# Kernel optimization log

Hardware: AMD Instinct MI355X
Metric: run time of the kernel (lower is better)

Reference implementation:

```python
import jax, jax.numpy as jnp
import numpy as np

NS, NT = 4000, 4096
E_S, E_T = 64000, 65536
D_IN, D_H, N_LAYERS = 128, 256, 3
SINK_ITERS = 10
EPS = 1e-10
ALPHA = 20.0


def scatter_mean(vals, idx, n):
    # torch_geometric aggr='mean': sum then divide by count (0 where count==0)
    s = jax.ops.segment_sum(vals, idx, num_segments=n)
    c = jax.ops.segment_sum(jnp.ones((idx.shape[0],), vals.dtype), idx, num_segments=n)
    return s / jnp.maximum(c, 1.0)[:, None]


def rel_cnn(x, edge_index, layers, final_w, final_b):
    # RelCNN(batch_norm=False, cat=True, lin=True), eval mode (dropout off)
    src, dst = edge_index[0], edge_index[1]
    n = x.shape[0]
    xs = [x]
    h = x
    for (w1, w2, wr, br) in layers:
        out1 = scatter_mean((h @ w1)[src], dst, n)  # source->target mean agg
        out2 = scatter_mean((h @ w2)[dst], src, n)  # target->source mean agg
        h = jax.nn.relu(h @ wr + br + out1 + out2)  # RelConv: root + out1 + out2
        xs.append(h)
    return jnp.concatenate(xs, axis=-1) @ final_w + final_b


def sinkhorn(S):
    # Sinkhorn(max_iter=10, eps=1e-10) with dummy_row=True, exp=True, alpha=20
    ns, nt = S.shape  # ns <= nt: pad dummy rows set to eps
    pad = jnp.full((nt - ns, nt), EPS, S.dtype)
    s = jnp.concatenate([S, pad], axis=0) + EPS
    s = jnp.exp(ALPHA * s)
    for i in range(SINK_ITERS):
        if i % 2 == 1:  # row normalization
            s = s / s.sum(axis=1, keepdims=True)
        else:           # column normalization
            s = s / s.sum(axis=0, keepdims=True)
    return s[:ns, :]  # drop dummy rows


def l2norm(x):
    return x / jnp.maximum(jnp.linalg.norm(x, axis=1, keepdims=True), 1e-12)


def setup_inputs() -> dict:
    key = jax.random.key(0)
    ks = jax.random.split(key, 20)
    d = {
        'x_s': jax.random.normal(ks[0], (NS, D_IN), jnp.float32),
        'x_t': jax.random.normal(ks[1], (NT, D_IN), jnp.float32),
        'edges': jax.random.randint(ks[2], (2, E_S), 0, NS, jnp.int32),
        'edget': jax.random.randint(ks[3], (2, E_T), 0, NT, jnp.int32),
    }
    k = 4
    fan = D_IN
    for l in range(N_LAYERS):
        sc = 1.0 / np.sqrt(fan)
        d[f'W1_{l}'] = jax.random.normal(ks[k], (fan, D_H), jnp.float32) * sc; k += 1
        d[f'W2_{l}'] = jax.random.normal(ks[k], (fan, D_H), jnp.float32) * sc; k += 1
        d[f'Wr_{l}'] = jax.random.normal(ks[k], (fan, D_H), jnp.float32) * sc; k += 1
        d[f'br_{l}'] = jax.random.normal(ks[k], (D_H,), jnp.float32) * 0.01; k += 1
        fan = D_H
    fin = D_IN + N_LAYERS * D_H
    d['final_w'] = jax.random.normal(ks[k], (fin, D_H), jnp.float32) * (0.01 / np.sqrt(fin)); k += 1
    d['final_b'] = jax.random.normal(ks[k], (D_H,), jnp.float32) * 0.001
    return d


def reference(x_s, x_t, edges, edget,
              W1_0, W2_0, Wr_0, br_0,
              W1_1, W2_1, Wr_1, br_1,
              W1_2, W2_2, Wr_2, br_2,
              final_w, final_b):
    layers = [(W1_0, W2_0, Wr_0, br_0), (W1_1, W2_1, Wr_1, br_1), (W1_2, W2_2, Wr_2, br_2)]
    h_s = rel_cnn(x_s, edges, layers, final_w, final_b)   # [NS, D_H]
    h_t = rel_cnn(x_t, edget, layers, final_w, final_b)   # [NT, D_H]
    match = l2norm(h_s) @ l2norm(h_t).T                   # [NS, NT]
    return sinkhorn(match)
```

## Files before the change

kernel.cpp:

```cpp
#include <hip/hip_runtime.h>
#include <hip/hip_bf16.h>

#define NS_N 4000
#define NT_N 4096
#define NTOT 8096
#define ES_E 64000
#define ET_E 65536
#define ETOT 129536
#define D_IN 128
#define D_H 256
#define CAT_D 896
#define TMP_D 768
#define NDUM (NT_N - NS_N)
#define ALPHA_F 20.0f
#define EPS_F 1e-10f

typedef __attribute__((ext_vector_type(8))) short bf16x8;
typedef __attribute__((ext_vector_type(4))) float f32x4;

__device__ inline short f2bf(float v) {
    __hip_bfloat16 b = __float2bfloat16(v);
    return *reinterpret_cast<short*>(&b);
}
__device__ inline float bf2f(short s) {
    __hip_bfloat16 b = *reinterpret_cast<__hip_bfloat16*>(&s);
    return __bfloat162float(b);
}
__device__ inline void splitf(float v, short& hi, short& lo) {
    hi = f2bf(v);
    lo = f2bf(v - bf2f(hi));
}

typedef __attribute__((address_space(1))) const char gas_t;
typedef __attribute__((address_space(3))) char las_t;
__device__ inline void gload16(const short* g, short* l) {
    __builtin_amdgcn_global_load_lds((gas_t*)g, (las_t*)l, 16, 0, 0);
}

template<int EPI>
__global__ __launch_bounds__(256) void mfma_gemm_kernel(
    const short* __restrict__ Ahi, const short* __restrict__ Alo,
    const short* __restrict__ Bhi, const short* __restrict__ Blo,
    const float* __restrict__ bias, float* __restrict__ C,
    int M, int N, int K, int lda, int ldb, int ldc)
{
    __shared__ short sAh[128 * 32];
    __shared__ short sAl[128 * 32];
    __shared__ short sBh[128 * 32];
    __shared__ short sBl[128 * 32];
    const int bm = blockIdx.x * 128;
    const int bn = blockIdx.y * 128;
    const int t = threadIdx.x;
    const int lane = t & 63, wv = t >> 6;
    const int wr = wv >> 1, wc = wv & 1;
    const int lr = lane & 15, lg = lane >> 4;

    f32x4 acc[4][4];
    #pragma unroll
    for (int i = 0; i < 4; ++i)
        #pragma unroll
        for (int j = 0; j < 4; ++j) {
            f32x4 z = {0.f, 0.f, 0.f, 0.f};
            acc[i][j] = z;
        }

    const int srow = lane >> 2, sseg = (lane & 3) * 8;

    for (int k0 = 0; k0 < K; k0 += 32) {
        auto stage = [&](const short* src, short* dst, int rowbase, int ld, int maxrow) {
            #pragma unroll
            for (int q = 0; q < 8; ++q) {
                int gr = min(rowbase + q * 16 + srow, maxrow);
                gload16(src + (size_t)gr * ld + k0 + sseg, dst + q * 512);
            }
        };
        if (wv == 0)      stage(Ahi, sAh, bm, lda, M - 1);
        else if (wv == 1) stage(Alo, sAl, bm, lda, M - 1);
        else if (wv == 2) stage(Bhi, sBh, bn, ldb, N - 1);
        else              stage(Blo, sBl, bn, ldb, N - 1);
        __syncthreads();

        bf16x8 ah[4], al[4], bh[4], bl[4];
        #pragma unroll
        for (int i = 0; i < 4; ++i) {
            int oa = (wr * 64 + i * 16 + lr) * 32 + lg * 8;
            ah[i] = *reinterpret_cast<const bf16x8*>(&sAh[oa]);
            al[i] = *reinterpret_cast<const bf16x8*>(&sAl[oa]);
            int ob = (wc * 64 + i * 16 + lr) * 32 + lg * 8;
            bh[i] = *reinterpret_cast<const bf16x8*>(&sBh[ob]);
            bl[i] = *reinterpret_cast<const bf16x8*>(&sBl[ob]);
        }
        #pragma unroll
        for (int i = 0; i < 4; ++i)
            #pragma unroll
            for (int j = 0; j < 4; ++j) {
                acc[i][j] = __builtin_amdgcn_mfma_f32_16x16x32_bf16(ah[i], bh[j], acc[i][j], 0, 0, 0);
                acc[i][j] = __builtin_amdgcn_mfma_f32_16x16x32_bf16(ah[i], bl[j], acc[i][j], 0, 0, 0);
                acc[i][j] = __builtin_amdgcn_mfma_f32_16x16x32_bf16(al[i], bh[j], acc[i][j], 0, 0, 0);
            }
        __syncthreads();
    }
    #pragma unroll
    for (int i = 0; i < 4; ++i) {
        #pragma unroll
        for (int j = 0; j < 4; ++j) {
            int col = bn + wc * 64 + j * 16 + lr;
            #pragma unroll
            for (int r = 0; r < 4; ++r) {
                int row = bm + wr * 64 + i * 16 + lg * 4 + r;
                if (row < M) {
                    float v = acc[i][j][r];
                    if (EPI == 1) v += bias[col];
                    if (EPI == 2) v = expf(ALPHA_F * (v + EPS_F));
                    C[(size_t)row * ldc + col] = v;
                }
            }
        }
    }
}

__global__ void wsplit3_kernel(const float* __restrict__ W1, const float* __restrict__ W2,
                               const float* __restrict__ Wr, short* __restrict__ WThi,
                               short* __restrict__ WTlo, int K)
{
    int idx = blockIdx.x * 256 + threadIdx.x;
    if (idx < K * TMP_D) {
        int k = idx / TMP_D, c = idx % TMP_D;
        float v = (c < 256) ? W1[k * 256 + c]
                : (c < 512) ? W2[k * 256 + (c - 256)]
                            : Wr[k * 256 + (c - 512)];
        short hi, lo;
        splitf(v, hi, lo);
        WThi[(size_t)c * K + k] = hi;
        WTlo[(size_t)c * K + k] = lo;
    }
}

__global__ void wsplitT_kernel(const float* __restrict__ W, short* __restrict__ WThi,
                               short* __restrict__ WTlo, int K, int Nw)
{
    int idx = blockIdx.x * 256 + threadIdx.x;
    if (idx < K * Nw) {
        int k = idx / Nw, n = idx % Nw;
        short hi, lo;
        splitf(W[idx], hi, lo);
        WThi[(size_t)n * K + k] = hi;
        WTlo[(size_t)n * K + k] = lo;
    }
}

__global__ void count2_kernel(const int* __restrict__ es, const int* __restrict__ et,
                              int* __restrict__ cin, int* __restrict__ cout)
{
    int e = blockIdx.x * 256 + threadIdx.x;
    int dir = blockIdx.y;
    int* cnt = dir ? cout : cin;
    if (e < ES_E) {
        int key = dir ? es[e] : es[e + ES_E];
        atomicAdd(&cnt[key], 1);
    } else if (e < ETOT) {
        int e2 = e - ES_E;
        int key = dir ? et[e2] : et[e2 + ET_E];
        atomicAdd(&cnt[key + NS_N], 1);
    }
}

__global__ __launch_bounds__(256) void scan2_kernel(const int* __restrict__ cin,
                                                    const int* __restrict__ cout,
                                                    int* __restrict__ rpin, int* __restrict__ rpout,
                                                    int* __restrict__ curin, int* __restrict__ curout)
{
    const int* cnt = blockIdx.x ? cout : cin;
    int* rowptr = blockIdx.x ? rpout : rpin;
    int* cur = blockIdx.x ? curout : curin;
    __shared__ int sums[256];
    const int t = threadIdx.x;
    const int per = (NTOT + 255) / 256;
    const int lo = t * per, hi = min((t + 1) * per, NTOT);
    int s = 0;
    for (int i = lo; i < hi; ++i) s += cnt[i];
    sums[t] = s;
    __syncthreads();
    for (int off = 1; off < 256; off <<= 1) {
        int v = (t >= off) ? sums[t - off] : 0;
        __syncthreads();
        sums[t] += v;
        __syncthreads();
    }
    int base = (t == 0) ? 0 : sums[t - 1];
    for (int i = lo; i < hi; ++i) { rowptr[i] = base; cur[i] = base; base += cnt[i]; }
    if (t == 255) rowptr[NTOT] = base;
}

__global__ void fill2_kernel(const int* __restrict__ es, const int* __restrict__ et,
                             int* __restrict__ curin, int* __restrict__ curout,
                             int* __restrict__ ciin, int* __restrict__ ciout)
{
    int e = blockIdx.x * 256 + threadIdx.x;
    int dir = blockIdx.y;
    int* cur = dir ? curout : curin;
    int* ci = dir ? ciout : ciin;
    int key, val, off;
    if (e < ES_E) {
        key = dir ? es[e] : es[e + ES_E];
        val = dir ? es[e + ES_E] : es[e];
        off = 0;
    } else if (e < ETOT) {
        int e2 = e - ES_E;
        key = dir ? et[e2] : et[e2 + ET_E];
        val = dir ? et[e2 + ET_E] : et[e2];
        off = NS_N;
    } else return;
    int pos = atomicAdd(&cur[key + off], 1);
    ci[pos] = val + off;
}

__global__ void copy_x_kernel(const float* __restrict__ xs, const float* __restrict__ xt,
                              short* __restrict__ CAThi, short* __restrict__ CATlo)
{
    int i = blockIdx.x, d = threadIdx.x;
    float v = (i < NS_N) ? xs[(size_t)i * D_IN + d] : xt[(size_t)(i - NS_N) * D_IN + d];
    short hi, lo;
    splitf(v, hi, lo);
    CAThi[(size_t)i * CAT_D + d] = hi;
    CATlo[(size_t)i * CAT_D + d] = lo;
}

__global__ __launch_bounds__(256) void gather_combine_kernel(
    const float* __restrict__ TMP,
    const int* __restrict__ rp_in, const int* __restrict__ ci_in,
    const int* __restrict__ rp_out, const int* __restrict__ ci_out,
    const float* __restrict__ br, short* __restrict__ CAThi, short* __restrict__ CATlo,
    int catoff)
{
    int node = blockIdx.x * 4 + (threadIdx.x >> 6);
    if (node >= NTOT) return;
    int d = (threadIdx.x & 63) * 4;

    float4 a1 = make_float4(0.f, 0.f, 0.f, 0.f);
    int b0 = rp_in[node], e0 = rp_in[node + 1];
    for (int e = b0; e < e0; ++e) {
        const float4 v = *reinterpret_cast<const float4*>(&TMP[(size_t)ci_in[e] * TMP_D + d]);
        a1.x += v.x; a1.y += v.y; a1.z += v.z; a1.w += v.w;
    }
    float s1 = 1.f / (float)max(e0 - b0, 1);

    float4 a2 = make_float4(0.f, 0.f, 0.f, 0.f);
    int b1 = rp_out[node], e1 = rp_out[node + 1];
    for (int e = b1; e < e1; ++e) {
        const float4 v = *reinterpret_cast<const float4*>(&TMP[(size_t)ci_out[e] * TMP_D + 256 + d]);
        a2.x += v.x; a2.y += v.y; a2.z += v.z; a2.w += v.w;
    }
    float s2 = 1.f / (float)max(e1 - b1, 1);

    const float4 rt = *reinterpret_cast<const float4*>(&TMP[(size_t)node * TMP_D + 512 + d]);
    const float4 bb = *reinterpret_cast<const float4*>(&br[d]);
    float o[4];
    o[0] = fmaxf(rt.x + bb.x + a1.x * s1 + a2.x * s2, 0.f);
    o[1] = fmaxf(rt.y + bb.y + a1.y * s1 + a2.y * s2, 0.f);
    o[2] = fmaxf(rt.z + bb.z + a1.z * s1 + a2.z * s2, 0.f);
    o[3] = fmaxf(rt.w + bb.w + a1.w * s1 + a2.w * s2, 0.f);
    short h[4], l[4];
    #pragma unroll
    for (int q = 0; q < 4; ++q) splitf(o[q], h[q], l[q]);
    *reinterpret_cast<short4*>(&CAThi[(size_t)node * CAT_D + catoff + d]) = make_short4(h[0], h[1], h[2], h[3]);
    *reinterpret_cast<short4*>(&CATlo[(size_t)node * CAT_D + catoff + d]) = make_short4(l[0], l[1], l[2], l[3]);
}

__global__ __launch_bounds__(256) void l2norm_kernel(const float* __restrict__ in,
                                                     short* __restrict__ outhi,
                                                     short* __restrict__ outlo, int N)
{
    int row = blockIdx.x * 4 + (threadIdx.x >> 6);
    if (row >= N) return;
    int d = (threadIdx.x & 63) * 4;
    float4 v = *reinterpret_cast<const float4*>(&in[(size_t)row * D_H + d]);
    float s = v.x * v.x + v.y * v.y + v.z * v.z + v.w * v.w;
    #pragma unroll
    for (int off = 32; off; off >>= 1) s += __shfl_xor(s, off);
    float inv = 1.f / fmaxf(sqrtf(s), 1e-12f);
    float o[4] = {v.x * inv, v.y * inv, v.z * inv, v.w * inv};
    short h[4], l[4];
    #pragma unroll
    for (int q = 0; q < 4; ++q) splitf(o[q], h[q], l[q]);
    *reinterpret_cast<short4*>(&outhi[(size_t)row * D_H + d]) = make_short4(h[0], h[1], h[2], h[3]);
    *reinterpret_cast<short4*>(&outlo[(size_t)row * D_H + d]) = make_short4(l[0], l[1], l[2], l[3]);
}

template<bool FIRST>
__global__ __launch_bounds__(256) void colsum_kernel(
    const float* __restrict__ s0, const float* __restrict__ r, float* __restrict__ tsum)
{
    int j4 = blockIdx.x * 256 + threadIdx.x;
    int i0 = blockIdx.y * 32;
    int iend = min(i0 + 32, NS_N);
    float4 s = make_float4(0.f, 0.f, 0.f, 0.f);
    for (int i = i0; i < iend; ++i) {
        float ri = FIRST ? 1.f : r[i];
        const float4 v = *reinterpret_cast<const float4*>(&s0[(size_t)i * NT_N + j4 * 4]);
        s.x += ri * v.x; s.y += ri * v.y; s.z += ri * v.z; s.w += ri * v.w;
    }
    atomicAdd(&tsum[j4 * 4 + 0], s.x);
    atomicAdd(&tsum[j4 * 4 + 1], s.y);
    atomicAdd(&tsum[j4 * 4 + 2], s.z);
    atomicAdd(&tsum[j4 * 4 + 3], s.w);
}

template<bool FIRST, bool FUSE_OUT>
__global__ __launch_bounds__(256) void rowsum_kernel(
    const float* __restrict__ s0, const float* __restrict__ tsum,
    const float* __restrict__ rdR, float* __restrict__ rdW,
    float* __restrict__ r, float* __restrict__ tsumNext,
    float* __restrict__ out, float dummyv)
{
    int i = blockIdx.x;
    int t = threadIdx.x;
    if (i < 16) tsumNext[i * 256 + t] = 0.f;
    float rdv = FIRST ? 1.f : rdR[0];
    float dd = (float)NDUM * dummyv * rdv;
    float s = 0.f;
    if (i < NS_N) {
        for (int j4 = t; j4 < NT_N / 4; j4 += 256) {
            const float4 v = *reinterpret_cast<const float4*>(&s0[(size_t)i * NT_N + j4 * 4]);
            const float4 ts = *reinterpret_cast<const float4*>(&tsum[j4 * 4]);
            s += v.x / (ts.x + dd) + v.y / (ts.y + dd) + v.z / (ts.z + dd) + v.w / (ts.w + dd);
        }
    } else {
        for (int j = t; j < NT_N; j += 256) s += 1.f / (tsum[j] + dd);
    }
    #pragma unroll
    for (int off = 32; off; off >>= 1) s += __shfl_xor(s, off);
    __shared__ float ws[4];
    __shared__ float ri_sh;
    if ((t & 63) == 0) ws[t >> 6] = s;
    __syncthreads();
    if (t == 0) {
        float tot = ws[0] + ws[1] + ws[2] + ws[3];
        if (i < NS_N) { r[i] = 1.f / tot; ri_sh = 1.f / tot; }
        else rdW[0] = 1.f / (dummyv * tot);
    }
    if (FUSE_OUT) {
        __syncthreads();
        if (i < NS_N) {
            float ri = ri_sh;
            for (int j4 = t; j4 < NT_N / 4; j4 += 256) {
                const float4 v = *reinterpret_cast<const float4*>(&s0[(size_t)i * NT_N + j4 * 4]);
                const float4 ts = *reinterpret_cast<const float4*>(&tsum[j4 * 4]);
                float4 o = make_float4(ri * v.x / (ts.x + dd), ri * v.y / (ts.y + dd),
                                       ri * v.z / (ts.z + dd), ri * v.w / (ts.w + dd));
                *reinterpret_cast<float4*>(&out[(size_t)i * NT_N + j4 * 4]) = o;
            }
        }
    }
}

extern "C" void kernel_launch(void* const* d_in, const int* in_sizes, int n_in,
                              void* d_out, int out_size, void* d_ws, size_t ws_size,
                              hipStream_t stream)
{
    const float* x_s = (const float*)d_in[0];
    const float* x_t = (const float*)d_in[1];
    const int* edges = (const int*)d_in[2];
    const int* edget = (const int*)d_in[3];
    const float* W1[3] = {(const float*)d_in[4], (const float*)d_in[8], (const float*)d_in[12]};
    const float* W2[3] = {(const float*)d_in[5], (const float*)d_in[9], (const float*)d_in[13]};
    const float* Wr[3] = {(const float*)d_in[6], (const float*)d_in[10], (const float*)d_in[14]};
    const float* br[3] = {(const float*)d_in[7], (const float*)d_in[11], (const float*)d_in[15]};
    const float* final_w = (const float*)d_in[16];
    const float* final_b = (const float*)d_in[17];
    float* out = (float*)d_out;

    float* W = (float*)d_ws;
    size_t off = 0;
    float* S0 = W + off;  off += (size_t)NS_N * NT_N;
    float* TMP = W + off; off += (size_t)NTOT * TMP_D;
    short* CAThi = (short*)(W + off); off += (size_t)NTOT * CAT_D / 2;
    short* CATlo = (short*)(W + off); off += (size_t)NTOT * CAT_D / 2;
    const int fan[3] = {D_IN, D_H, D_H};
    short* WThi[3]; short* WTlo[3];
    for (int l = 0; l < 3; ++l) {
        WThi[l] = (short*)(W + off); off += (size_t)TMP_D * fan[l] / 2;
        WTlo[l] = (short*)(W + off); off += (size_t)TMP_D * fan[l] / 2;
    }
    short* WFhi = (short*)(W + off); off += (size_t)D_H * CAT_D / 2;
    short* WFlo = (short*)(W + off); off += (size_t)D_H * CAT_D / 2;
    float* RVEC = W + off; off += NS_N;
    float* RD   = W + off; off += 8;
    float* TSA  = W + off; off += NT_N;
    int* CNT_IN  = (int*)(W + off); off += NTOT;
    int* CNT_OUT = (int*)(W + off); off += NTOT;
    float* TSB  = W + off; off += NT_N;
    int* RP_IN   = (int*)(W + off); off += NTOT + 1;
    int* RP_OUT  = (int*)(W + off); off += NTOT + 3;
    int* CUR_IN  = (int*)(W + off); off += NTOT;
    int* CUR_OUT = (int*)(W + off); off += NTOT;
    int* CI_IN   = (int*)(W + off); off += ETOT;
    int* CI_OUT  = (int*)(W + off); off += ETOT;
    float* HFIN = TMP;
    short* HNhi = (short*)(TMP + (size_t)NTOT * D_H);
    short* HNlo = (short*)(TMP + (size_t)NTOT * D_H + (size_t)NTOT * D_H / 2);

    const int cat_off[4] = {0, 128, 384, 640};

    hipMemsetAsync(TSA, 0, (NT_N + 2 * NTOT) * sizeof(int), stream);

    for (int l = 0; l < 3; ++l)
        wsplit3_kernel<<<(fan[l] * TMP_D + 255) / 256, 256, 0, stream>>>(
            W1[l], W2[l], Wr[l], WThi[l], WTlo[l], fan[l]);
    wsplitT_kernel<<<(CAT_D * D_H + 255) / 256, 256, 0, stream>>>(final_w, WFhi, WFlo, CAT_D, D_H);

    {
        dim3 gc((ETOT + 255) / 256, 2);
        count2_kernel<<<gc, 256, 0, stream>>>(edges, edget, CNT_IN, CNT_OUT);
        scan2_kernel<<<2, 256, 0, stream>>>(CNT_IN, CNT_OUT, RP_IN, RP_OUT, CUR_IN, CUR_OUT);
        fill2_kernel<<<gc, 256, 0, stream>>>(edges, edget, CUR_IN, CUR_OUT, CI_IN, CI_OUT);
    }

    copy_x_kernel<<<NTOT, 128, 0, stream>>>(x_s, x_t, CAThi, CATlo);

    for (int l = 0; l < 3; ++l) {
        dim3 gg((NTOT + 127) / 128, TMP_D / 128);
        mfma_gemm_kernel<0><<<gg, 256, 0, stream>>>(
            CAThi + cat_off[l], CATlo + cat_off[l], WThi[l], WTlo[l], nullptr, TMP,
            NTOT, TMP_D, fan[l], CAT_D, fan[l], TMP_D);
        gather_combine_kernel<<<(NTOT + 3) / 4, 256, 0, stream>>>(
            TMP, RP_IN, CI_IN, RP_OUT, CI_OUT, br[l], CAThi, CATlo, cat_off[l + 1]);
    }

    {
        dim3 gf((NTOT + 127) / 128, D_H / 128);
        mfma_gemm_kernel<1><<<gf, 256, 0, stream>>>(
            CAThi, CATlo, WFhi, WFlo, final_b, HFIN, NTOT, D_H, CAT_D, CAT_D, CAT_D, D_H);
        l2norm_kernel<<<(NTOT + 3) / 4, 256, 0, stream>>>(HFIN, HNhi, HNlo, NTOT);
    }

    {
        dim3 gm((NS_N + 127) / 128, NT_N / 128);
        mfma_gemm_kernel<2><<<gm, 256, 0, stream>>>(
            HNhi, HNlo, HNhi + (size_t)NS_N * D_H, HNlo + (size_t)NS_N * D_H, nullptr, S0,
            NS_N, NT_N, D_H, D_H, D_H, NT_N);
    }

    const float dummyv = expf(ALPHA_F * (EPS_F + EPS_F));
    dim3 gcs(NT_N / 1024, (NS_N + 31) / 32);
    colsum_kernel<true><<<gcs, 256, 0, stream>>>(S0, nullptr, TSA);
    rowsum_kernel<true, false><<<NS_N + 1, 256, 0, stream>>>(
        S0, TSA, nullptr, &RD[0], RVEC, TSB, nullptr, dummyv);
    colsum_kernel<false><<<gcs, 256, 0, stream>>>(S0, RVEC, TSB);
    rowsum_kernel<false, false><<<NS_N + 1, 256, 0, stream>>>(
        S0, TSB, &RD[0], &RD[1], RVEC, TSA, nullptr, dummyv);
    colsum_kernel<false><<<gcs, 256, 0, stream>>>(S0, RVEC, TSA);
    rowsum_kernel<false, false><<<NS_N + 1, 256, 0, stream>>>(
        S0, TSA, &RD[1], &RD[0], RVEC, TSB, nullptr, dummyv);
    colsum_kernel<false><<<gcs, 256, 0, stream>>>(S0, RVEC, TSB);
    rowsum_kernel<false, false><<<NS_N + 1, 256, 0, stream>>>(
        S0, TSB, &RD[0], &RD[1], RVEC, TSA, nullptr, dummyv);
    colsum_kernel<false><<<gcs, 256, 0, stream>>>(S0, RVEC, TSA);
    rowsum_kernel<false, true><<<NS_N + 1, 256, 0, stream>>>(
        S0, TSA, &RD[1], &RD[0], RVEC, TSB, out, dummyv);
}
```

Baseline: 627.3 us.

## Double-buffer GEMM LDS, fuse first Sinkhorn column sum, merge prep kernels

```diff
diff --git a/kernel.cpp b/kernel.cpp
--- a/kernel.cpp
+++ b/kernel.cpp
@@ -37,23 +37,25 @@
     __builtin_amdgcn_global_load_lds((gas_t*)g, (las_t*)l, 16, 0, 0);
 }
 
-template<int EPI>
+template<int EPI, bool COLSUM>
 __global__ __launch_bounds__(256) void mfma_gemm_kernel(
     const short* __restrict__ Ahi, const short* __restrict__ Alo,
     const short* __restrict__ Bhi, const short* __restrict__ Blo,
     const float* __restrict__ bias, float* __restrict__ C,
+    float* __restrict__ colacc,
     int M, int N, int K, int lda, int ldb, int ldc)
 {
-    __shared__ short sAh[128 * 32];
-    __shared__ short sAl[128 * 32];
-    __shared__ short sBh[128 * 32];
-    __shared__ short sBl[128 * 32];
+    __shared__ __align__(16) short sAh[2][4096];
+    __shared__ __align__(16) short sAl[2][4096];
+    __shared__ __align__(16) short sBh[2][4096];
+    __shared__ __align__(16) short sBl[2][4096];
     const int bm = blockIdx.x * 128;
     const int bn = blockIdx.y * 128;
-    const int t = threadIdx.x;
-    const int lane = t & 63, wv = t >> 6;
+    const int tid = threadIdx.x;
+    const int lane = tid & 63, wv = tid >> 6;
     const int wr = wv >> 1, wc = wv & 1;
     const int lr = lane & 15, lg = lane >> 4;
+    const int srow = lane >> 2, sseg = (lane & 3) * 8;
 
     f32x4 acc[4][4];
     #pragma unroll
@@ -64,31 +66,34 @@
             acc[i][j] = z;
         }
 
-    const int srow = lane >> 2, sseg = (lane & 3) * 8;
-
-    for (int k0 = 0; k0 < K; k0 += 32) {
-        auto stage = [&](const short* src, short* dst, int rowbase, int ld, int maxrow) {
-            #pragma unroll
-            for (int q = 0; q < 8; ++q) {
-                int gr = min(rowbase + q * 16 + srow, maxrow);
-                gload16(src + (size_t)gr * ld + k0 + sseg, dst + q * 512);
-            }
-        };
-        if (wv == 0)      stage(Ahi, sAh, bm, lda, M - 1);
-        else if (wv == 1) stage(Alo, sAl, bm, lda, M - 1);
-        else if (wv == 2) stage(Bhi, sBh, bn, ldb, N - 1);
-        else              stage(Blo, sBl, bn, ldb, N - 1);
-        __syncthreads();
-
+    auto stage = [&](int buf, int k0) {
+        const short* src; short* dst; int rowbase, ld, maxrow;
+        if (wv == 0)      { src = Ahi; dst = &sAh[buf][0]; rowbase = bm; ld = lda; maxrow = M - 1; }
+        else if (wv == 1) { src = Alo; dst = &sAl[buf][0]; rowbase = bm; ld = lda; maxrow = M - 1; }
+        else if (wv == 2) { src = Bhi; dst = &sBh[buf][0]; rowbase = bn; ld = ldb; maxrow = N - 1; }
+        else              { src = Blo; dst = &sBl[buf][0]; rowbase = bn; ld = ldb; maxrow = N - 1; }
+        #pragma unroll
+        for (int q = 0; q < 8; ++q) {
+            int gr = min(rowbase + q * 16 + srow, maxrow);
+            gload16(src + (size_t)gr * ld + k0 + sseg, dst + q * 512);
+        }
+    };
+
+    stage(0, 0);
+    __syncthreads();
+    int cur = 0;
+    const int NTILES = K >> 5;
+    for (int t0 = 0; t0 < NTILES; ++t0) {
+        if (t0 + 1 < NTILES) stage(cur ^ 1, (t0 + 1) << 5);
         bf16x8 ah[4], al[4], bh[4], bl[4];
         #pragma unroll
         for (int i = 0; i < 4; ++i) {
             int oa = (wr * 64 + i * 16 + lr) * 32 + lg * 8;
-            ah[i] = *reinterpret_cast<const bf16x8*>(&sAh[oa]);
-            al[i] = *reinterpret_cast<const bf16x8*>(&sAl[oa]);
+            ah[i] = *reinterpret_cast<const bf16x8*>(&sAh[cur][oa]);
+            al[i] = *reinterpret_cast<const bf16x8*>(&sAl[cur][oa]);
             int ob = (wc * 64 + i * 16 + lr) * 32 + lg * 8;
-            bh[i] = *reinterpret_cast<const bf16x8*>(&sBh[ob]);
-            bl[i] = *reinterpret_cast<const bf16x8*>(&sBl[ob]);
+            bh[i] = *reinterpret_cast<const bf16x8*>(&sBh[cur][ob]);
+            bl[i] = *reinterpret_cast<const bf16x8*>(&sBl[cur][ob]);
         }
         #pragma unroll
         for (int i = 0; i < 4; ++i)
@@ -99,32 +104,65 @@
                 acc[i][j] = __builtin_amdgcn_mfma_f32_16x16x32_bf16(al[i], bh[j], acc[i][j], 0, 0, 0);
             }
         __syncthreads();
-    }
+        cur ^= 1;
+    }
+
+    float colp[4] = {0.f, 0.f, 0.f, 0.f};
     #pragma unroll
     for (int i = 0; i < 4; ++i) {
         #pragma unroll
         for (int j = 0; j < 4; ++j) {
             int col = bn + wc * 64 + j * 16 + lr;
             #pragma unroll
-            for (int r = 0; r < 4; ++r) {
-                int row = bm + wr * 64 + i * 16 + lg * 4 + r;
+            for (int rr = 0; rr < 4; ++rr) {
+                int row = bm + wr * 64 + i * 16 + lg * 4 + rr;
                 if (row < M) {
-                    float v = acc[i][j][r];
+                    float v = acc[i][j][rr];
                     if (EPI == 1) v += bias[col];
                     if (EPI == 2) v = expf(ALPHA_F * (v + EPS_F));
                     C[(size_t)row * ldc + col] = v;
+                    if (COLSUM) colp[j] += v;
                 }
             }
         }
     }
-}
-
-__global__ void wsplit3_kernel(const float* __restrict__ W1, const float* __restrict__ W2,
-                               const float* __restrict__ Wr, short* __restrict__ WThi,
-                               short* __restrict__ WTlo, int K)
-{
-    int idx = blockIdx.x * 256 + threadIdx.x;
-    if (idx < K * TMP_D) {
+    if (COLSUM) {
+        #pragma unroll
+        for (int j = 0; j < 4; ++j) {
+            float v = colp[j];
+            v += __shfl_xor(v, 16);
+            v += __shfl_xor(v, 32);
+            if (lg == 0) atomicAdd(&colacc[bn + wc * 64 + j * 16 + lr], v);
+        }
+    }
+}
+
+__global__ __launch_bounds__(256) void prep_kernel(
+    const float* __restrict__ xs, const float* __restrict__ xt,
+    const float* __restrict__ W1a, const float* __restrict__ W2a, const float* __restrict__ Wra,
+    const float* __restrict__ W1b, const float* __restrict__ W2b, const float* __restrict__ Wrb,
+    const float* __restrict__ W1c, const float* __restrict__ W2c, const float* __restrict__ Wrc,
+    const float* __restrict__ WF,
+    short* __restrict__ WThi0, short* __restrict__ WTlo0,
+    short* __restrict__ WThi1, short* __restrict__ WTlo1,
+    short* __restrict__ WThi2, short* __restrict__ WTlo2,
+    short* __restrict__ WFhi, short* __restrict__ WFlo,
+    short* __restrict__ CAThi, short* __restrict__ CATlo,
+    int* __restrict__ zbase)
+{
+    int blk = blockIdx.x;
+    const int t = threadIdx.x;
+    if (blk < 80) {
+        int idx = blk * 256 + t;
+        if (idx < NT_N + 2 * NTOT) zbase[idx] = 0;
+        return;
+    }
+    blk -= 80;
+    if (blk < 384 + 768 + 768) {
+        const float *W1, *W2, *Wr; short *WThi, *WTlo; int K, idx;
+        if (blk < 384)      { W1 = W1a; W2 = W2a; Wr = Wra; WThi = WThi0; WTlo = WTlo0; K = 128; idx = blk * 256 + t; }
+        else if (blk < 1152){ W1 = W1b; W2 = W2b; Wr = Wrb; WThi = WThi1; WTlo = WTlo1; K = 256; idx = (blk - 384) * 256 + t; }
+        else                { W1 = W1c; W2 = W2c; Wr = Wrc; WThi = WThi2; WTlo = WTlo2; K = 256; idx = (blk - 1152) * 256 + t; }
         int k = idx / TMP_D, c = idx % TMP_D;
         float v = (c < 256) ? W1[k * 256 + c]
                 : (c < 512) ? W2[k * 256 + (c - 256)]
@@ -133,19 +171,27 @@
         splitf(v, hi, lo);
         WThi[(size_t)c * K + k] = hi;
         WTlo[(size_t)c * K + k] = lo;
-    }
-}
-
-__global__ void wsplitT_kernel(const float* __restrict__ W, short* __restrict__ WThi,
-                               short* __restrict__ WTlo, int K, int Nw)
-{
-    int idx = blockIdx.x * 256 + threadIdx.x;
-    if (idx < K * Nw) {
-        int k = idx / Nw, n = idx % Nw;
+        return;
+    }
+    blk -= 1920;
+    if (blk < 896) {
+        int idx = blk * 256 + t;
+        int k = idx / D_H, n = idx % D_H;
         short hi, lo;
-        splitf(W[idx], hi, lo);
-        WThi[(size_t)n * K + k] = hi;
-        WTlo[(size_t)n * K + k] = lo;
+        splitf(WF[idx], hi, lo);
+        WFhi[(size_t)n * CAT_D + k] = hi;
+        WFlo[(size_t)n * CAT_D + k] = lo;
+        return;
+    }
+    blk -= 896;
+    {
+        int idx = blk * 256 + t;
+        int i = idx >> 7, d = idx & 127;
+        float v = (i < NS_N) ? xs[(size_t)i * D_IN + d] : xt[(size_t)(i - NS_N) * D_IN + d];
+        short hi, lo;
+        splitf(v, hi, lo);
+        CAThi[(size_t)i * CAT_D + d] = hi;
+        CATlo[(size_t)i * CAT_D + d] = lo;
     }
 }
 
@@ -215,17 +261,6 @@
     ci[pos] = val + off;
 }
 
-__global__ void copy_x_kernel(const float* __restrict__ xs, const float* __restrict__ xt,
-                              short* __restrict__ CAThi, short* __restrict__ CATlo)
-{
-    int i = blockIdx.x, d = threadIdx.x;
-    float v = (i < NS_N) ? xs[(size_t)i * D_IN + d] : xt[(size_t)(i - NS_N) * D_IN + d];
-    short hi, lo;
-    splitf(v, hi, lo);
-    CAThi[(size_t)i * CAT_D + d] = hi;
-    CATlo[(size_t)i * CAT_D + d] = lo;
-}
-
 __global__ __launch_bounds__(256) void gather_combine_kernel(
     const float* __restrict__ TMP,
     const int* __restrict__ rp_in, const int* __restrict__ ci_in,
@@ -287,7 +322,6 @@
     *reinterpret_cast<short4*>(&outlo[(size_t)row * D_H + d]) = make_short4(l[0], l[1], l[2], l[3]);
 }
 
-template<bool FIRST>
 __global__ __launch_bounds__(256) void colsum_kernel(
     const float* __restrict__ s0, const float* __restrict__ r, float* __restrict__ tsum)
 {
@@ -296,7 +330,7 @@
     int iend = min(i0 + 32, NS_N);
     float4 s = make_float4(0.f, 0.f, 0.f, 0.f);
     for (int i = i0; i < iend; ++i) {
-        float ri = FIRST ? 1.f : r[i];
+        float ri = r[i];
         const float4 v = *reinterpret_cast<const float4*>(&s0[(size_t)i * NT_N + j4 * 4]);
         s.x += ri * v.x; s.y += ri * v.y; s.z += ri * v.z; s.w += ri * v.w;
     }
@@ -402,12 +436,11 @@
 
     const int cat_off[4] = {0, 128, 384, 640};
 
-    hipMemsetAsync(TSA, 0, (NT_N + 2 * NTOT) * sizeof(int), stream);
-
-    for (int l = 0; l < 3; ++l)
-        wsplit3_kernel<<<(fan[l] * TMP_D + 255) / 256, 256, 0, stream>>>(
-            W1[l], W2[l], Wr[l], WThi[l], WTlo[l], fan[l]);
-    wsplitT_kernel<<<(CAT_D * D_H + 255) / 256, 256, 0, stream>>>(final_w, WFhi, WFlo, CAT_D, D_H);
+    prep_kernel<<<6944, 256, 0, stream>>>(
+        x_s, x_t,
+        W1[0], W2[0], Wr[0], W1[1], W2[1], Wr[1], W1[2], W2[2], Wr[2], final_w,
+        WThi[0], WTlo[0], WThi[1], WTlo[1], WThi[2], WTlo[2], WFhi, WFlo,
+        CAThi, CATlo, (int*)TSA);
 
     {
         dim3 gc((ETOT + 255) / 256, 2);
@@ -416,12 +449,10 @@
         fill2_kernel<<<gc, 256, 0, stream>>>(edges, edget, CUR_IN, CUR_OUT, CI_IN, CI_OUT);
     }
 
-    copy_x_kernel<<<NTOT, 128, 0, stream>>>(x_s, x_t, CAThi, CATlo);
-
     for (int l = 0; l < 3; ++l) {
         dim3 gg((NTOT + 127) / 128, TMP_D / 128);
-        mfma_gemm_kernel<0><<<gg, 256, 0, stream>>>(
-            CAThi + cat_off[l], CATlo + cat_off[l], WThi[l], WTlo[l], nullptr, TMP,
+        mfma_gemm_kernel<0, false><<<gg, 256, 0, stream>>>(
+            CAThi + cat_off[l], CATlo + cat_off[l], WThi[l], WTlo[l], nullptr, TMP, nullptr,
             NTOT, TMP_D, fan[l], CAT_D, fan[l], TMP_D);
         gather_combine_kernel<<<(NTOT + 3) / 4, 256, 0, stream>>>(
             TMP, RP_IN, CI_IN, RP_OUT, CI_OUT, br[l], CAThi, CATlo, cat_off[l + 1]);
@@ -429,33 +460,33 @@
 
     {
         dim3 gf((NTOT + 127) / 128, D_H / 128);
-        mfma_gemm_kernel<1><<<gf, 256, 0, stream>>>(
-            CAThi, CATlo, WFhi, WFlo, final_b, HFIN, NTOT, D_H, CAT_D, CAT_D, CAT_D, D_H);
+        mfma_gemm_kernel<1, false><<<gf, 256, 0, stream>>>(
+            CAThi, CATlo, WFhi, WFlo, final_b, HFIN, nullptr,
+            NTOT, D_H, CAT_D, CAT_D, CAT_D, D_H);
         l2norm_kernel<<<(NTOT + 3) / 4, 256, 0, stream>>>(HFIN, HNhi, HNlo, NTOT);
     }
 
     {
         dim3 gm((NS_N + 127) / 128, NT_N / 128);
-        mfma_gemm_kernel<2><<<gm, 256, 0, stream>>>(
-            HNhi, HNlo, HNhi + (size_t)NS_N * D_H, HNlo + (size_t)NS_N * D_H, nullptr, S0,
+        mfma_gemm_kernel<2, true><<<gm, 256, 0, stream>>>(
+            HNhi, HNlo, HNhi + (size_t)NS_N * D_H, HNlo + (size_t)NS_N * D_H, nullptr, S0, TSA,
             NS_N, NT_N, D_H, D_H, D_H, NT_N);
     }
 
     const float dummyv = expf(ALPHA_F * (EPS_F + EPS_F));
     dim3 gcs(NT_N / 1024, (NS_N + 31) / 32);
-    colsum_kernel<true><<<gcs, 256, 0, stream>>>(S0, nullptr, TSA);
     rowsum_kernel<true, false><<<NS_N + 1, 256, 0, stream>>>(
         S0, TSA, nullptr, &RD[0], RVEC, TSB, nullptr, dummyv);
-    colsum_kernel<false><<<gcs, 256, 0, stream>>>(S0, RVEC, TSB);
+    colsum_kernel<<<gcs, 256, 0, stream>>>(S0, RVEC, TSB);
     rowsum_kernel<false, false><<<NS_N + 1, 256, 0, stream>>>(
         S0, TSB, &RD[0], &RD[1], RVEC, TSA, nullptr, dummyv);
-    colsum_kernel<false><<<gcs, 256, 0, stream>>>(S0, RVEC, TSA);
+    colsum_kernel<<<gcs, 256, 0, stream>>>(S0, RVEC, TSA);
     rowsum_kernel<false, false><<<NS_N + 1, 256, 0, stream>>>(
         S0, TSA, &RD[1], &RD[0], RVEC, TSB, nullptr, dummyv);
-    colsum_kernel<false><<<gcs, 256, 0, stream>>>(S0, RVEC, TSB);
+    colsum_kernel<<<gcs, 256, 0, stream>>>(S0, RVEC, TSB);
     rowsum_kernel<false, false><<<NS_N + 1, 256, 0, stream>>>(
         S0, TSB, &RD[0], &RD[1], RVEC, TSA, nullptr, dummyv);
-    colsum_kernel<false><<<gcs, 256, 0, stream>>>(S0, RVEC, TSA);
+    colsum_kernel<<<gcs, 256, 0, stream>>>(S0, RVEC, TSA);
     rowsum_kernel<false, true><<<NS_N + 1, 256, 0, stream>>>(
         S0, TSA, &RD[1], &RD[0], RVEC, TSB, out, dummyv);
 }
```

Result: faster. 580.4 us (-7.5%).
